# Optimization experiments

Hardware: AMD Instinct MI355X
Metric: run time of the kernel (lower is better)

Reference implementation:

```python
import jax, jax.numpy as jnp
import numpy as np

B, T, D, H = 2, 2048, 1024, 16
HD = D // H
SCALE = HD ** -0.5
NEG_INF = float(np.finfo(np.float32).min)


def setup_inputs() -> dict:
    key = jax.random.key(0)
    ks = jax.random.split(key, 10)
    s = 1.0 / np.sqrt(D)
    x = jax.random.normal(ks[0], (B, T, D), dtype=jnp.float32)
    # causal mask, True = keep, shape (B,1,T,T)
    mask = jnp.broadcast_to(jnp.tril(jnp.ones((T, T), dtype=bool)), (B, 1, T, T))
    Wq = jax.random.normal(ks[1], (D, D), dtype=jnp.float32) * s
    bq = jax.random.normal(ks[2], (D,), dtype=jnp.float32) * s
    Wk = jax.random.normal(ks[3], (D, D), dtype=jnp.float32) * s
    bk = jax.random.normal(ks[4], (D,), dtype=jnp.float32) * s
    Wv = jax.random.normal(ks[5], (D, D), dtype=jnp.float32) * s
    bv = jax.random.normal(ks[6], (D,), dtype=jnp.float32) * s
    Wo = jax.random.normal(ks[7], (D, D), dtype=jnp.float32) * s
    bo = jax.random.normal(ks[8], (D,), dtype=jnp.float32) * s
    return {"x": x, "mask": mask, "Wq": Wq, "bq": bq, "Wk": Wk, "bk": bk,
            "Wv": Wv, "bv": bv, "Wo": Wo, "bo": bo}


def _split_heads(t):
    # (B,T,D) -> (B,H,T,HD)
    return t.reshape(B, T, H, HD).transpose(0, 2, 1, 3)


def masked_rowwise_softmax(scores, mask):
    # mask: bool, True = keep; fully-masked rows return zeros.
    s = scores.astype(jnp.float32)
    masked = jnp.where(mask, s, NEG_INF)
    row_max = jnp.max(masked, axis=-1, keepdims=True)
    exps = jnp.exp(masked - row_max) * mask.astype(jnp.float32)
    denom = jnp.maximum(jnp.sum(exps, axis=-1, keepdims=True), 1e-12)
    return (exps / denom).astype(scores.dtype)


def reference(x, mask, Wq, bq, Wk, bk, Wv, bv, Wo, bo):
    q = _split_heads(x @ Wq.T + bq)
    k = _split_heads(x @ Wk.T + bk)
    v = _split_heads(x @ Wv.T + bv)
    scores = jnp.einsum('bhqd,bhkd->bhqk', q, k) * SCALE
    m = jnp.broadcast_to(mask, (B, H, T, T))
    attn = masked_rowwise_softmax(scores, m)
    y = jnp.einsum('bhqk,bhkd->bhqd', attn, v)
    y = y.transpose(0, 2, 1, 3).reshape(B, T, D)
    return y @ Wo.T + bo
```

## Files before the change

kernel.cpp:

```cpp
#include <hip/hip_runtime.h>

#define B_ 2
#define H_ 16
#define T_ 2048
#define D_ 1024
#define HD_ 64
#define NEG_HUGE (-3.402823466e38f)
#define QSCALE 0.18033688011112042f

typedef unsigned short u16;
typedef unsigned int u32;
typedef __attribute__((ext_vector_type(8))) short bf16x8;
typedef __attribute__((ext_vector_type(4))) float f32x4;
typedef __attribute__((ext_vector_type(4))) u32 u32x4;

typedef const __attribute__((address_space(1))) void* gas_t;
typedef __attribute__((address_space(3))) void* las_t;

__device__ __forceinline__ u16 f2bf(float f) {
    u32 u = __builtin_bit_cast(u32, f);
    u += 0x7FFFu + ((u >> 16) & 1u);
    return (u16)(u >> 16);
}

__device__ __forceinline__ u32 pk2bf(float f0, float f1) {
    const u32 a0 = __builtin_bit_cast(u32, f0) + 0x8000u;
    const u32 a1 = __builtin_bit_cast(u32, f1) + 0x8000u;
    return __builtin_amdgcn_perm(a1, a0, 0x07060302u);
}

__device__ __forceinline__ u32 cvtpk2bf(float f0, float f1) {
    u32 r;
    asm("v_cvt_pk_bf16_f32 %0, %1, %2" : "=v"(r) : "v"(f0), "v"(f1));
    return r;
}

__device__ __forceinline__ uint2 pk4bf(f32x4 a) {
    uint2 r;
    r.x = pk2bf(a[0], a[1]);
    r.y = pk2bf(a[2], a[3]);
    return r;
}

__device__ __forceinline__ f32x4 mfma16(bf16x8 a, bf16x8 b, f32x4 c) {
    return __builtin_amdgcn_mfma_f32_16x16x32_bf16(a, b, c, 0, 0, 0);
}

__global__ __launch_bounds__(256) void to_bf16(
    const float* __restrict__ x,  const float* __restrict__ wq,
    const float* __restrict__ wk, const float* __restrict__ wv,
    const float* __restrict__ wo, u16* __restrict__ dst)
{
    const size_t g = ((size_t)blockIdx.x * 256 + threadIdx.x) * 8;
    const float* src; size_t off;
    if      (g < (size_t)(4u << 20)) { src = x;  off = g; }
    else if (g < (size_t)(5u << 20)) { src = wq; off = g - (size_t)(4u << 20); }
    else if (g < (size_t)(6u << 20)) { src = wk; off = g - (size_t)(5u << 20); }
    else if (g < (size_t)(7u << 20)) { src = wv; off = g - (size_t)(6u << 20); }
    else                             { src = wo; off = g - (size_t)(7u << 20); }
    const float4 a = *(const float4*)&src[off];
    const float4 b = *(const float4*)&src[off + 4];
    ushort4 lo = make_ushort4(f2bf(a.x), f2bf(a.y), f2bf(a.z), f2bf(a.w));
    ushort4 hi = make_ushort4(f2bf(b.x), f2bf(b.y), f2bf(b.z), f2bf(b.w));
    *(ushort4*)&dst[g]     = lo;
    *(ushort4*)&dst[g + 4] = hi;
}

__device__ __forceinline__ void gemm128_core(
    const u16* __restrict__ P0, const u16* __restrict__ P1,
    const int m0, const int n0, u16* As, u16* Bs, f32x4 (&acc)[4][4])
{
    const int tid  = threadIdx.x;
    const int lane = tid & 63;
    const int quad = lane >> 4;
    const int l15  = lane & 15;
    const int w    = tid >> 6;
    const int wm   = (w >> 1) << 6;
    const int wn   = (w & 1) << 6;
    const int swz  = l15 & 7;

    size_t aoff[4], boff[4];
    int    loff[4];
#pragma unroll
    for (int i = 0; i < 4; ++i) {
        const int slot = i * 256 + tid;
        const int r = slot >> 3, c = slot & 7;
        const int gc = (c ^ (r & 7)) << 3;
        aoff[i] = (size_t)(m0 + r) * D_ + gc;
        boff[i] = (size_t)(n0 + r) * D_ + gc;
        loff[i] = slot * 8;
    }
    int rowA[4], rowB[4];
#pragma unroll
    for (int i = 0; i < 4; ++i) {
        rowA[i] = (wm + i * 16 + l15) * 64;
        rowB[i] = (wn + i * 16 + l15) * 64;
    }

    bf16x8 pa[4], pb[4];
#pragma unroll
    for (int i = 0; i < 4; ++i) {
        pa[i] = *(const bf16x8*)&P0[aoff[i]];
        pb[i] = *(const bf16x8*)&P1[boff[i]];
    }

    for (int k0 = 0; k0 < D_; k0 += 64) {
        __syncthreads();
#pragma unroll
        for (int i = 0; i < 4; ++i) {
            *(bf16x8*)&As[loff[i]] = pa[i];
            *(bf16x8*)&Bs[loff[i]] = pb[i];
        }
        if (k0 + 64 < D_) {
            const int kn = k0 + 64;
#pragma unroll
            for (int i = 0; i < 4; ++i) {
                pa[i] = *(const bf16x8*)&P0[aoff[i] + kn];
                pb[i] = *(const bf16x8*)&P1[boff[i] + kn];
            }
        }
        __syncthreads();
#pragma unroll
        for (int s = 0; s < 2; ++s) {
            const int ch = (((s << 2) + quad) ^ swz) << 3;
            bf16x8 am[4], bm[4];
#pragma unroll
            for (int mi = 0; mi < 4; ++mi) am[mi] = *(const bf16x8*)&As[rowA[mi] + ch];
#pragma unroll
            for (int ni = 0; ni < 4; ++ni) bm[ni] = *(const bf16x8*)&Bs[rowB[ni] + ch];
#pragma unroll
            for (int mi = 0; mi < 4; ++mi)
#pragma unroll
                for (int ni = 0; ni < 4; ++ni)
                    acc[mi][ni] = mfma16(am[mi], bm[ni], acc[mi][ni]);
        }
    }
}

__global__ __launch_bounds__(512, 2) void gemm_qkv(
    const u16* __restrict__ xb,
    const u16* __restrict__ Wqb, const u16* __restrict__ Wkb, const u16* __restrict__ Wvb,
    const float* __restrict__ bq, const float* __restrict__ bk, const float* __restrict__ bv,
    u16* __restrict__ Qb, u16* __restrict__ Kb, u16* __restrict__ Vtb)
{
    __shared__ u16 lds[65536];
    const int tid  = threadIdx.x;
    const int lane = tid & 63;
    const int quad = lane >> 4;
    const int l15  = lane & 15;
    const int w    = tid >> 6;
    const int wr   = w >> 2;
    const int wc   = w & 3;
    const int swz7 = l15 & 7;

    const int L  = blockIdx.x;
    const int wg = (L & 7) * 24 + (L >> 3);
    const int ftile = wg >> 4;
    const int ttile = wg & 15;
    const int z  = ftile >> 2;
    const int fb = (ftile & 3) << 8;

    const u16* PA; const u16* PB;
    int Ra, Rb;
    if (z == 0)      { PA = Wqb; PB = xb;  Ra = fb;         Rb = ttile << 8; }
    else if (z == 1) { PA = Wkb; PB = xb;  Ra = fb;         Rb = ttile << 8; }
    else             { PA = xb;  PB = Wvb; Ra = ttile << 8; Rb = fb;         }

    const int rr  = tid >> 3;
    const int cc8 = ((tid & 7) ^ (rr & 7)) << 3;
    size_t srcA[4], srcB[4];
#pragma unroll
    for (int i = 0; i < 4; ++i) {
        srcA[i] = (size_t)(Ra + i * 64 + rr) * D_ + cc8;
        srcB[i] = (size_t)(Rb + i * 64 + rr) * D_ + cc8;
    }
    const int dstT = tid * 8;

#define QKV_STAGE(p, kt) do {                                               \
    const size_t ko_ = (size_t)(kt) * 64;                                   \
    _Pragma("unroll")                                                       \
    for (int i_ = 0; i_ < 4; ++i_)                                          \
        __builtin_amdgcn_global_load_lds((gas_t)(PA + srcA[i_] + ko_),      \
            (las_t)&lds[((p) << 14) + i_ * 4096 + dstT], 16, 0, 0);         \
    _Pragma("unroll")                                                       \
    for (int i_ = 0; i_ < 4; ++i_)                                          \
        __builtin_amdgcn_global_load_lds((gas_t)(PB + srcB[i_] + ko_),      \
            (las_t)&lds[32768 + ((p) << 14) + i_ * 4096 + dstT], 16, 0, 0); \
} while (0)

    const int baseA = ((wr << 7) + l15) * 64;
    const int baseB = 32768 + ((wc << 6) + l15) * 64;
    const int cs0 = (quad ^ swz7) << 3;
    const int cs1 = ((quad + 4) ^ swz7) << 3;

    f32x4 acc[8][4];
#pragma unroll
    for (int i = 0; i < 8; ++i)
#pragma unroll
        for (int j = 0; j < 4; ++j) acc[i][j] = (f32x4){0.f, 0.f, 0.f, 0.f};

    QKV_STAGE(0, 0);
    QKV_STAGE(1, 1);
    asm volatile("s_waitcnt vmcnt(8)" ::: "memory");
    __builtin_amdgcn_s_barrier();

    for (int kt = 0; kt < 16; ++kt) {
        const int pO = (kt & 1) << 14;
        bf16x8 bfr[4][2], afr[4][2];
#pragma unroll
        for (int ni = 0; ni < 4; ++ni) {
            bfr[ni][0] = *(const bf16x8*)&lds[pO + baseB + ni * 1024 + cs0];
            bfr[ni][1] = *(const bf16x8*)&lds[pO + baseB + ni * 1024 + cs1];
        }
#pragma unroll
        for (int mi = 0; mi < 4; ++mi) {
            afr[mi][0] = *(const bf16x8*)&lds[pO + baseA + mi * 1024 + cs0];
            afr[mi][1] = *(const bf16x8*)&lds[pO + baseA + mi * 1024 + cs1];
        }
        __builtin_amdgcn_s_setprio(1);
#pragma unroll
        for (int mi = 0; mi < 4; ++mi)
#pragma unroll
            for (int ni = 0; ni < 4; ++ni) {
                acc[mi][ni] = mfma16(afr[mi][0], bfr[ni][0], acc[mi][ni]);
                acc[mi][ni] = mfma16(afr[mi][1], bfr[ni][1], acc[mi][ni]);
            }
        __builtin_amdgcn_s_setprio(0);
#pragma unroll
        for (int mi = 0; mi < 4; ++mi) {
            afr[mi][0] = *(const bf16x8*)&lds[pO + baseA + (mi + 4) * 1024 + cs0];
            afr[mi][1] = *(const bf16x8*)&lds[pO + baseA + (mi + 4) * 1024 + cs1];
        }
        asm volatile("s_waitcnt lgkmcnt(0)" ::: "memory");
        __builtin_amdgcn_sched_barrier(0);
        __builtin_amdgcn_s_barrier();
        __builtin_amdgcn_sched_barrier(0);
        if (kt + 2 < 16) QKV_STAGE(kt & 1, kt + 2);
        __builtin_amdgcn_s_setprio(1);
#pragma unroll
        for (int mi = 0; mi < 4; ++mi)
#pragma unroll
            for (int ni = 0; ni < 4; ++ni) {
                acc[mi + 4][ni] = mfma16(afr[mi][0], bfr[ni][0], acc[mi + 4][ni]);
                acc[mi + 4][ni] = mfma16(afr[mi][1], bfr[ni][1], acc[mi + 4][ni]);
            }
        __builtin_amdgcn_s_setprio(0);
        if (kt < 14) asm volatile("s_waitcnt vmcnt(8)" ::: "memory");
        else         asm volatile("s_waitcnt vmcnt(0)" ::: "memory");
        __builtin_amdgcn_sched_barrier(0);
        __builtin_amdgcn_s_barrier();
    }
#undef QKV_STAGE

    __syncthreads();
    u16* scr = &lds[w * 8192];
    const int pq   = quad >> 1;
    const int psub = (quad & 1) << 2;

    if (z < 2) {
        const float* bias = (z == 0) ? bq : bk;
        const float  CF   = (z == 0) ? QSCALE : 1.f;
        u16*         Cq   = (z == 0) ? Qb : Kb;
        const int fbw = fb + (wr << 7);
        const int tbw = (ttile << 8) + (wc << 6);
#pragma unroll
        for (int mi = 0; mi < 8; ++mi) {
            const float4 bi = *(const float4*)&bias[fbw + mi * 16 + (quad << 2)];
            const int c = (mi << 1) + pq;
#pragma unroll
            for (int ni = 0; ni < 4; ++ni) {
                const int tl = ni * 16 + l15;
                f32x4 a = acc[mi][ni];
                f32x4 v = { (a[0] + bi.x) * CF, (a[1] + bi.y) * CF,
                            (a[2] + bi.z) * CF, (a[3] + bi.w) * CF };
                *(uint2*)&scr[tl * 128 + ((c ^ (tl & 15)) << 3) + psub] = pk4bf(v);
            }
        }
        __asm__ volatile("s_waitcnt lgkmcnt(0)" ::: "memory");
        const int hb = fbw >> 6;
#pragma unroll
        for (int e = 0; e < 16; ++e) {
            const int tl = (e << 2) + (lane >> 4);
            const int c  = lane & 15;
            bf16x8 v = *(const bf16x8*)&scr[tl * 128 + ((c ^ (tl & 15)) << 3)];
            const int tg = tbw + tl;
            const int bb = tg >> 11, t0 = tg & 2047;
            *(bf16x8*)&Cq[((size_t)((bb << 4) + hb + (c >> 3)) * T_ + t0) * HD_ +
                          ((c & 7) << 3)] = v;
        }
    } else {
        const int fvw = fb + (wc << 6);
        const int h   = fvw >> 6;
        const int tbw = (ttile << 8) + (wr << 7);
#pragma unroll
        for (int ni = 0; ni < 4; ++ni) {
            const int hdrow = ni * 16 + l15;
            const float bi = bv[fvw + ni * 16 + l15];
            const int sw = hdrow & 15;
#pragma unroll
            for (int mi = 0; mi < 8; ++mi) {
                f32x4 a = acc[mi][ni];
                f32x4 v = { a[0] + bi, a[1] + bi, a[2] + bi, a[3] + bi };
                const int c = (mi << 1) + pq;
                *(uint2*)&scr[hdrow * 128 + ((c ^ sw) << 3) + psub] = pk4bf(v);
            }
        }
        __asm__ volatile("s_waitcnt lgkmcnt(0)" ::: "memory");
#pragma unroll
        for (int e = 0; e < 16; ++e) {
            const int hdl = (e << 2) + (lane >> 4);
            const int c   = lane & 15;
            bf16x8 v = *(const bf16x8*)&scr[hdl * 128 + ((c ^ (hdl & 15)) << 3)];
            const int tg = tbw + (c << 3);
            const int bb = tg >> 11, t0 = tg & 2047;
            *(bf16x8*)&Vtb[((size_t)((bb << 4) + h) * HD_ + hdl) * T_ + t0] = v;
        }
    }
}

__global__ __launch_bounds__(256) void gemm_out(
    const u16* __restrict__ Ab, const u16* __restrict__ Wob,
    const float* __restrict__ bo, float* __restrict__ C)
{
    __shared__ u16 As[128 * 64];
    __shared__ u16 Bs[128 * 64];
    const int L   = blockIdx.x;
    const int xcd = L & 7;
    const int kk  = L >> 3;
    const int tt  = (xcd << 2) + (kk & 3);
    const int ft  = kk >> 2;
    const int m0  = tt << 7;
    const int n0  = ft << 7;

    f32x4 acc[4][4];
#pragma unroll
    for (int i = 0; i < 4; ++i)
#pragma unroll
        for (int j = 0; j < 4; ++j) acc[i][j] = (f32x4){0.f, 0.f, 0.f, 0.f};

    gemm128_core(Ab, Wob, m0, n0, As, Bs, acc);

    const int tid  = threadIdx.x;
    const int lane = tid & 63;
    const int quad = lane >> 4;
    const int l15  = lane & 15;
    const int w    = tid >> 6;
    const int wm   = (w >> 1) << 6;
    const int wn   = (w & 1) << 6;

    float bi[4];
#pragma unroll
    for (int ni = 0; ni < 4; ++ni) bi[ni] = bo[n0 + wn + ni * 16 + l15];

#pragma unroll
    for (int mi = 0; mi < 4; ++mi) {
        const int m = m0 + wm + mi * 16 + (quad << 2);
#pragma unroll
        for (int r = 0; r < 4; ++r)
#pragma unroll
            for (int ni = 0; ni < 4; ++ni)
                C[(size_t)(m + r) * D_ + n0 + wn + ni * 16 + l15] = acc[mi][ni][r] + bi[ni];
    }
}

__global__ __launch_bounds__(256) void attn_mfma(
    const u16* __restrict__ Qg, const u16* __restrict__ Kg,
    const u16* __restrict__ Vtg, u16* __restrict__ Out)
{
    __shared__ u16 Ks[128 * 64];
    __shared__ u16 Vs[64 * 128];
    const int tid  = threadIdx.x;
    const int w    = tid >> 6;
    const int lane = tid & 63;
    const int quad = lane >> 4;
    const int l15  = lane & 15;
    const int bh   = blockIdx.x;
    const int qt   = 31 - (int)blockIdx.y;
    const size_t base = (size_t)bh * (T_ * HD_);

    int lK[4], lV[4];
    size_t gK[4], gV[4];
#pragma unroll
    for (int i = 0; i < 4; ++i) {
        const int slot = i * 256 + tid;
        const int rk = slot >> 3, ck = slot & 7;
        lK[i] = rk * 64 + ((ck ^ (rk & 7)) << 3);
        gK[i] = base + (size_t)rk * HD_ + ck * 8;
        const int rv = slot >> 4, cv = slot & 15;
        lV[i] = rv * 128 + ((cv ^ (rv & 15)) << 3);
        gV[i] = base + (size_t)rv * T_ + cv * 8;
    }

    bf16x8 ones;
#pragma unroll
    for (int i = 0; i < 8; ++i) ones[i] = (short)0x3F80;

    const int swz7 = l15 & 7;
    const int b = bh >> 4, h = bh & 15;

    const int qloc = (w << 4) + l15;
    const int qrow = (qt << 6) + qloc;
    const bf16x8 qf0 = *(const bf16x8*)&Qg[base + (size_t)qrow * HD_ + quad * 8];
    const bf16x8 qf1 = *(const bf16x8*)&Qg[base + (size_t)qrow * HD_ + 32 + quad * 8];

    f32x4 o[4];
#pragma unroll
    for (int nt = 0; nt < 4; ++nt) o[nt] = (f32x4){0.f, 0.f, 0.f, 0.f};
    f32x4 Lacc = (f32x4){0.f, 0.f, 0.f, 0.f};

    const int nIter = (qt + 2) >> 1;
    bf16x8 kreg[4], vreg[4];
#pragma unroll
    for (int i = 0; i < 4; ++i) {
        kreg[i] = *(const bf16x8*)&Kg[gK[i]];
        vreg[i] = *(const bf16x8*)&Vtg[gV[i]];
    }

    for (int it = 0; it < nIter; ++it) {
        __syncthreads();
#pragma unroll
        for (int i = 0; i < 4; ++i) {
            *(bf16x8*)&Ks[lK[i]] = kreg[i];
            *(bf16x8*)&Vs[lV[i]] = vreg[i];
        }
        if (it + 1 < nIter) {
            const int koff = (it + 1) << 7;
#pragma unroll
            for (int i = 0; i < 4; ++i) {
                kreg[i] = *(const bf16x8*)&Kg[gK[i] + (size_t)koff * HD_];
                vreg[i] = *(const bf16x8*)&Vtg[gV[i] + koff];
            }
        }
        __syncthreads();

        f32x4 st[8];
#pragma unroll
        for (int t = 0; t < 8; ++t) {
            const int kr = (t * 16 + l15) * 64;
            const bf16x8 k0 = *(const bf16x8*)&Ks[kr + ((quad ^ swz7) << 3)];
            const bf16x8 k1 = *(const bf16x8*)&Ks[kr + (((quad + 4) ^ swz7) << 3)];
            f32x4 a = (f32x4){0.f, 0.f, 0.f, 0.f};
            a = mfma16(k0, qf0, a);
            a = mfma16(k1, qf1, a);
            st[t] = a;
        }

        if (it == nIter - 1) {
            const int koff = it << 7;
#pragma unroll
            for (int t = 0; t < 8; ++t)
#pragma unroll
                for (int r = 0; r < 4; ++r) {
                    const int kg = koff + t * 16 + (quad << 2) + r;
                    if (kg > qrow) st[t][r] = NEG_HUGE;
                }
        }

#pragma unroll
        for (int t = 0; t < 8; ++t)
#pragma unroll
            for (int r = 0; r < 4; ++r) st[t][r] = __builtin_amdgcn_exp2f(st[t][r]);

        bf16x8 pf[4];
#pragma unroll
        for (int kq = 0; kq < 4; ++kq) {
            u32 c00 = cvtpk2bf(st[2 * kq][0],     st[2 * kq][1]);
            u32 c01 = cvtpk2bf(st[2 * kq][2],     st[2 * kq][3]);
            u32 c10 = cvtpk2bf(st[2 * kq + 1][0], st[2 * kq + 1][1]);
            u32 c11 = cvtpk2bf(st[2 * kq + 1][2], st[2 * kq + 1][3]);
            asm("v_permlane32_swap_b32 %0, %1" : "+v"(c00), "+v"(c10));
            asm("v_permlane16_swap_b32 %0, %1" : "+v"(c00), "+v"(c10));
            asm("v_permlane32_swap_b32 %0, %1" : "+v"(c01), "+v"(c11));
            asm("v_permlane16_swap_b32 %0, %1" : "+v"(c01), "+v"(c11));
            u32x4 dw;
            dw[0] = c00; dw[1] = c01; dw[2] = c10; dw[3] = c11;
            pf[kq] = __builtin_bit_cast(bf16x8, dw);
        }

        __builtin_amdgcn_s_setprio(1);
#pragma unroll
        for (int nt = 0; nt < 4; ++nt) {
            f32x4 oo = o[nt];
            const int vr = (nt * 16 + l15) * 128;
#pragma unroll
            for (int kq = 0; kq < 4; ++kq) {
                const bf16x8 vf = *(const bf16x8*)&Vs[vr + ((((kq << 2) + quad) ^ l15) << 3)];
                oo = mfma16(pf[kq], vf, oo);
            }
            o[nt] = oo;
        }
#pragma unroll
        for (int kq = 0; kq < 4; ++kq)
            Lacc = mfma16(pf[kq], ones, Lacc);
        __builtin_amdgcn_s_setprio(0);
    }

    f32x4 linv;
#pragma unroll
    for (int r = 0; r < 4; ++r) linv[r] = 1.f / fmaxf(Lacc[r], 1e-30f);

#pragma unroll
    for (int nt = 0; nt < 4; ++nt)
#pragma unroll
        for (int r = 0; r < 4; ++r) {
            const int qg2 = (qt << 6) + (w << 4) + (quad << 2) + r;
            const u32 u = __builtin_bit_cast(u32, o[nt][r] * linv[r]) + 0x8000u;
            Out[(size_t)(b * T_ + qg2) * D_ + (h << 6) + nt * 16 + l15] = (u16)(u >> 16);
        }
}

extern "C" void kernel_launch(void* const* d_in, const int* in_sizes, int n_in,
                              void* d_out, int out_size, void* d_ws, size_t ws_size,
                              hipStream_t stream)
{
    const float* x  = (const float*)d_in[0];
    const float* Wq = (const float*)d_in[2];
    const float* bq = (const float*)d_in[3];
    const float* Wk = (const float*)d_in[4];
    const float* bk = (const float*)d_in[5];
    const float* Wv = (const float*)d_in[6];
    const float* bv = (const float*)d_in[7];
    const float* Wo = (const float*)d_in[8];
    const float* bo = (const float*)d_in[9];
    float* out = (float*)d_out;

    const size_t M1 = (size_t)1 << 20;
    u16* wsu = (u16*)d_ws;
    u16* xb  = wsu;
    u16* wqb = wsu + 4 * M1;
    u16* wkb = wsu + 5 * M1;
    u16* wvb = wsu + 6 * M1;
    u16* wob = wsu + 7 * M1;
    u16* Qb  = wsu + 8 * M1;
    u16* Kb  = wsu + 12 * M1;
    u16* Vtb = wsu + 16 * M1;
    u16* AOb = wsu + 20 * M1;

    to_bf16<<<4096, 256, 0, stream>>>(x, Wq, Wk, Wv, Wo, wsu);

    gemm_qkv<<<192, 512, 0, stream>>>(xb, wqb, wkb, wvb, bq, bk, bv, Qb, Kb, Vtb);

    dim3 ga(B_ * H_, T_ / 64);
    attn_mfma<<<ga, 256, 0, stream>>>(Qb, Kb, Vtb, AOb);

    gemm_out<<<256, 256, 0, stream>>>(AOb, wob, bo, out);
}
```

Before: 187.0 us.

## Split attention keys across warp pairs with 2x2 query/key warp tiling

Reorganizes the four warps of the attention kernel into a 2x2 grid. Each warp now handles 32 query rows against half of the 128-key tile, where before each warp handled 16 query rows against all keys. Each K and V fragment read from shared memory is reused across two query subtiles, which cuts LDS traffic per MFMA. The cost is a final cross-warp reduction of partial outputs and row sums through shared memory, plus higher register pressure from doubled accumulators.

```diff
diff --git a/kernel.cpp b/kernel.cpp
--- a/kernel.cpp
+++ b/kernel.cpp
@@ -378,6 +378,10 @@
     const int qt   = 31 - (int)blockIdx.y;
     const size_t base = (size_t)bh * (T_ * HD_);
 
+    const int qw   = w >> 1;
+    const int kw   = w & 1;
+    const int wkey = kw << 6;
+
     int lK[4], lV[4];
     size_t gK[4], gV[4];
 #pragma unroll
@@ -398,15 +402,23 @@
     const int swz7 = l15 & 7;
     const int b = bh >> 4, h = bh & 15;
 
-    const int qloc = (w << 4) + l15;
-    const int qrow = (qt << 6) + qloc;
-    const bf16x8 qf0 = *(const bf16x8*)&Qg[base + (size_t)qrow * HD_ + quad * 8];
-    const bf16x8 qf1 = *(const bf16x8*)&Qg[base + (size_t)qrow * HD_ + 32 + quad * 8];
-
-    f32x4 o[4];
-#pragma unroll
-    for (int nt = 0; nt < 4; ++nt) o[nt] = (f32x4){0.f, 0.f, 0.f, 0.f};
-    f32x4 Lacc = (f32x4){0.f, 0.f, 0.f, 0.f};
+    bf16x8 qf[2][2];
+#pragma unroll
+    for (int j = 0; j < 2; ++j) {
+        const size_t qoff =
+            base + (size_t)((qt << 6) + (qw << 5) + j * 16 + l15) * HD_ + quad * 8;
+        qf[j][0] = *(const bf16x8*)&Qg[qoff];
+        qf[j][1] = *(const bf16x8*)&Qg[qoff + 32];
+    }
+
+    f32x4 o[2][4];
+#pragma unroll
+    for (int j = 0; j < 2; ++j)
+#pragma unroll
+        for (int nt = 0; nt < 4; ++nt) o[j][nt] = (f32x4){0.f, 0.f, 0.f, 0.f};
+    f32x4 Lacc[2];
+    Lacc[0] = (f32x4){0.f, 0.f, 0.f, 0.f};
+    Lacc[1] = (f32x4){0.f, 0.f, 0.f, 0.f};
 
     const int nIter = (qt + 2) >> 1;
     bf16x8 kreg[4], vreg[4];
@@ -433,80 +445,134 @@
         }
         __syncthreads();
 
-        f32x4 st[8];
-#pragma unroll
-        for (int t = 0; t < 8; ++t) {
-            const int kr = (t * 16 + l15) * 64;
+        f32x4 st[4][2];
+#pragma unroll
+        for (int mt = 0; mt < 4; ++mt) {
+            const int kr = (wkey + mt * 16 + l15) * 64;
             const bf16x8 k0 = *(const bf16x8*)&Ks[kr + ((quad ^ swz7) << 3)];
             const bf16x8 k1 = *(const bf16x8*)&Ks[kr + (((quad + 4) ^ swz7) << 3)];
-            f32x4 a = (f32x4){0.f, 0.f, 0.f, 0.f};
-            a = mfma16(k0, qf0, a);
-            a = mfma16(k1, qf1, a);
-            st[t] = a;
+#pragma unroll
+            for (int j = 0; j < 2; ++j) {
+                f32x4 a = (f32x4){0.f, 0.f, 0.f, 0.f};
+                a = mfma16(k0, qf[j][0], a);
+                a = mfma16(k1, qf[j][1], a);
+                st[mt][j] = a;
+            }
         }
 
         if (it == nIter - 1) {
-            const int koff = it << 7;
-#pragma unroll
-            for (int t = 0; t < 8; ++t)
+            const int kb = (it << 7) + wkey;
+#pragma unroll
+            for (int mt = 0; mt < 4; ++mt)
 #pragma unroll
                 for (int r = 0; r < 4; ++r) {
-                    const int kg = koff + t * 16 + (quad << 2) + r;
-                    if (kg > qrow) st[t][r] = NEG_HUGE;
+                    const int kg = kb + mt * 16 + (quad << 2) + r;
+#pragma unroll
+                    for (int j = 0; j < 2; ++j) {
+                        const int qg = (qt << 6) + (qw << 5) + j * 16 + l15;
+                        if (kg > qg) st[mt][j][r] = NEG_HUGE;
+                    }
                 }
         }
 
 #pragma unroll
-        for (int t = 0; t < 8; ++t)
-#pragma unroll
-            for (int r = 0; r < 4; ++r) st[t][r] = __builtin_amdgcn_exp2f(st[t][r]);
-
-        bf16x8 pf[4];
-#pragma unroll
-        for (int kq = 0; kq < 4; ++kq) {
-            u32 c00 = cvtpk2bf(st[2 * kq][0],     st[2 * kq][1]);
-            u32 c01 = cvtpk2bf(st[2 * kq][2],     st[2 * kq][3]);
-            u32 c10 = cvtpk2bf(st[2 * kq + 1][0], st[2 * kq + 1][1]);
-            u32 c11 = cvtpk2bf(st[2 * kq + 1][2], st[2 * kq + 1][3]);
-            asm("v_permlane32_swap_b32 %0, %1" : "+v"(c00), "+v"(c10));
-            asm("v_permlane16_swap_b32 %0, %1" : "+v"(c00), "+v"(c10));
-            asm("v_permlane32_swap_b32 %0, %1" : "+v"(c01), "+v"(c11));
-            asm("v_permlane16_swap_b32 %0, %1" : "+v"(c01), "+v"(c11));
-            u32x4 dw;
-            dw[0] = c00; dw[1] = c01; dw[2] = c10; dw[3] = c11;
-            pf[kq] = __builtin_bit_cast(bf16x8, dw);
-        }
+        for (int mt = 0; mt < 4; ++mt)
+#pragma unroll
+            for (int j = 0; j < 2; ++j)
+#pragma unroll
+                for (int r = 0; r < 4; ++r)
+                    st[mt][j][r] = __builtin_amdgcn_exp2f(st[mt][j][r]);
+
+        bf16x8 pf[2][2];
+#pragma unroll
+        for (int kq = 0; kq < 2; ++kq)
+#pragma unroll
+            for (int j = 0; j < 2; ++j) {
+                u32 c00 = cvtpk2bf(st[2 * kq][j][0],     st[2 * kq][j][1]);
+                u32 c01 = cvtpk2bf(st[2 * kq][j][2],     st[2 * kq][j][3]);
+                u32 c10 = cvtpk2bf(st[2 * kq + 1][j][0], st[2 * kq + 1][j][1]);
+                u32 c11 = cvtpk2bf(st[2 * kq + 1][j][2], st[2 * kq + 1][j][3]);
+                asm("v_permlane32_swap_b32 %0, %1" : "+v"(c00), "+v"(c10));
+                asm("v_permlane16_swap_b32 %0, %1" : "+v"(c00), "+v"(c10));
+                asm("v_permlane32_swap_b32 %0, %1" : "+v"(c01), "+v"(c11));
+                asm("v_permlane16_swap_b32 %0, %1" : "+v"(c01), "+v"(c11));
+                u32x4 dw;
+                dw[0] = c00; dw[1] = c01; dw[2] = c10; dw[3] = c11;
+                pf[kq][j] = __builtin_bit_cast(bf16x8, dw);
+            }
 
         __builtin_amdgcn_s_setprio(1);
 #pragma unroll
         for (int nt = 0; nt < 4; ++nt) {
-            f32x4 oo = o[nt];
             const int vr = (nt * 16 + l15) * 128;
 #pragma unroll
-            for (int kq = 0; kq < 4; ++kq) {
-                const bf16x8 vf = *(const bf16x8*)&Vs[vr + ((((kq << 2) + quad) ^ l15) << 3)];
-                oo = mfma16(pf[kq], vf, oo);
-            }
-            o[nt] = oo;
-        }
-#pragma unroll
-        for (int kq = 0; kq < 4; ++kq)
-            Lacc = mfma16(pf[kq], ones, Lacc);
+            for (int kq = 0; kq < 2; ++kq) {
+                const bf16x8 vf = *(const bf16x8*)
+                    &Vs[vr + ((((kw << 3) + (kq << 2) + quad) ^ l15) << 3)];
+#pragma unroll
+                for (int j = 0; j < 2; ++j)
+                    o[j][nt] = mfma16(pf[kq][j], vf, o[j][nt]);
+            }
+        }
+#pragma unroll
+        for (int kq = 0; kq < 2; ++kq)
+#pragma unroll
+            for (int j = 0; j < 2; ++j)
+                Lacc[j] = mfma16(pf[kq][j], ones, Lacc[j]);
         __builtin_amdgcn_s_setprio(0);
     }
 
-    f32x4 linv;
-#pragma unroll
-    for (int r = 0; r < 4; ++r) linv[r] = 1.f / fmaxf(Lacc[r], 1e-30f);
-
-#pragma unroll
-    for (int nt = 0; nt < 4; ++nt)
-#pragma unroll
-        for (int r = 0; r < 4; ++r) {
-            const int qg2 = (qt << 6) + (w << 4) + (quad << 2) + r;
-            const u32 u = __builtin_bit_cast(u32, o[nt][r] * linv[r]) + 0x8000u;
-            Out[(size_t)(b * T_ + qg2) * D_ + (h << 6) + nt * 16 + l15] = (u16)(u >> 16);
-        }
+    __syncthreads();
+    float* Rf = (float*)Ks;
+    float* Lf = (float*)Vs;
+    if (kw == 1) {
+#pragma unroll
+        for (int j = 0; j < 2; ++j) {
+#pragma unroll
+            for (int nt = 0; nt < 4; ++nt)
+#pragma unroll
+                for (int r = 0; r < 4; ++r)
+                    Rf[(qw << 11) + (j * 16 + (quad << 2) + r) * 64 + nt * 16 + l15]
+                        = o[j][nt][r];
+            if (l15 == 0) {
+#pragma unroll
+                for (int r = 0; r < 4; ++r)
+                    Lf[(qw << 5) + j * 16 + (quad << 2) + r] = Lacc[j][r];
+            }
+        }
+    }
+    __syncthreads();
+    if (kw == 0) {
+#pragma unroll
+        for (int j = 0; j < 2; ++j) {
+#pragma unroll
+            for (int nt = 0; nt < 4; ++nt)
+#pragma unroll
+                for (int r = 0; r < 4; ++r)
+                    o[j][nt][r] +=
+                        Rf[(qw << 11) + (j * 16 + (quad << 2) + r) * 64 + nt * 16 + l15];
+#pragma unroll
+            for (int r = 0; r < 4; ++r)
+                Lacc[j][r] += Lf[(qw << 5) + j * 16 + (quad << 2) + r];
+        }
+
+#pragma unroll
+        for (int j = 0; j < 2; ++j) {
+            f32x4 linv;
+#pragma unroll
+            for (int r = 0; r < 4; ++r) linv[r] = 1.f / fmaxf(Lacc[j][r], 1e-30f);
+#pragma unroll
+            for (int nt = 0; nt < 4; ++nt)
+#pragma unroll
+                for (int r = 0; r < 4; ++r) {
+                    const int qg2 = (qt << 6) + (qw << 5) + j * 16 + (quad << 2) + r;
+                    const u32 u =
+                        __builtin_bit_cast(u32, o[j][nt][r] * linv[r]) + 0x8000u;
+                    Out[(size_t)(b * T_ + qg2) * D_ + (h << 6) + nt * 16 + l15]
+                        = (u16)(u >> 16);
+                }
+        }
+    }
 }
 
 extern "C" void kernel_launch(void* const* d_in, const int* in_sizes, int n_in,
```

After: 189.4 us. No clear change (+1.3%).
